# Performance work log

Measured on AMD Instinct MI355X. Metric: run time of the kernel, lower is better.

## Reference

```python
import jax, jax.numpy as jnp
import numpy as np

IMG = 64
NZ = 100
ENC_H = 800
DEC_H = 1600
IN_SZ = IMG * IMG  # 4096
D_ENC_IN = 2 * IN_SZ * 3 + DEC_H  # 26176


def setup_inputs() -> dict:
    key = jax.random.key(0)
    ks = jax.random.split(key, 12)
    B, T = 64, 10
    s = 0.02  # weight init scale to keep gates in sane range
    return {
        "x": jax.random.uniform(ks[0], (B, 3, IMG, IMG), jnp.float32),
        "noise": jax.random.normal(ks[1], (T, B, NZ), jnp.float32),
        "W_ih_mu": jax.random.normal(ks[2], (4 * ENC_H, D_ENC_IN), jnp.float32) * s,
        "W_hh_mu": jax.random.normal(ks[3], (4 * ENC_H, ENC_H), jnp.float32) * s,
        "b_mu": jnp.zeros((4 * ENC_H,), jnp.float32),
        "W_ih_lv": jax.random.normal(ks[4], (4 * ENC_H, D_ENC_IN), jnp.float32) * s,
        "W_hh_lv": jax.random.normal(ks[5], (4 * ENC_H, ENC_H), jnp.float32) * s,
        "b_lv": jnp.zeros((4 * ENC_H,), jnp.float32),
        "W_mu_fc": jax.random.normal(ks[6], (NZ, ENC_H), jnp.float32) * s,
        "b_mu_fc": jnp.zeros((NZ,), jnp.float32),
        "W_lv_fc": jax.random.normal(ks[7], (NZ, ENC_H), jnp.float32) * s,
        "b_lv_fc": jnp.zeros((NZ,), jnp.float32),
        "W_ih_dec": jax.random.normal(ks[8], (4 * DEC_H, NZ), jnp.float32) * s,
        "W_hh_dec": jax.random.normal(ks[9], (4 * DEC_H, DEC_H), jnp.float32) * s,
        "b_dec": jnp.zeros((4 * DEC_H,), jnp.float32),
        "W_write": jax.random.normal(ks[10], (3 * IN_SZ, DEC_H), jnp.float32) * s,
        "b_write": jnp.zeros((3 * IN_SZ,), jnp.float32),
        "T": T,
    }


def _lstm_cell(xin, h, c, W_ih, W_hh, b):
    # torch LSTMCell: gates ordered i, f, g, o
    g = xin @ W_ih.T + h @ W_hh.T + b
    i, f, gg, o = jnp.split(g, 4, axis=1)
    c_new = jax.nn.sigmoid(f) * c + jax.nn.sigmoid(i) * jnp.tanh(gg)
    h_new = jax.nn.sigmoid(o) * jnp.tanh(c_new)
    return h_new, c_new


def reference(x, noise, W_ih_mu, W_hh_mu, b_mu, W_ih_lv, W_hh_lv, b_lv,
              W_mu_fc, b_mu_fc, W_lv_fc, b_lv_fc,
              W_ih_dec, W_hh_dec, b_dec, W_write, b_write, T):
    B = x.shape[0]
    x_flat = x.reshape(B, -1)  # [B, 3*64*64]
    init = (
        jnp.zeros((B, 3, IMG, IMG), x.dtype),   # canvas c
        jnp.zeros((B, ENC_H), x.dtype), jnp.zeros((B, ENC_H), x.dtype),  # h_mu, c_mu
        jnp.zeros((B, ENC_H), x.dtype), jnp.zeros((B, ENC_H), x.dtype),  # h_lv, c_lv
        jnp.zeros((B, DEC_H), x.dtype), jnp.zeros((B, DEC_H), x.dtype),  # h_dec, c_dec
    )

    def step(carry, eps):
        c, h_mu, c_mu, h_lv, c_lv, h_dec, c_dec = carry
        sb = jax.nn.sigmoid(c)
        x_hat = (x - sb).reshape(B, -1)
        enc_in = jnp.concatenate([x_flat, x_hat, h_dec], axis=1)  # [B, 26176]
        h_mu, c_mu = _lstm_cell(enc_in, h_mu, c_mu, W_ih_mu, W_hh_mu, b_mu)
        mu = jax.nn.relu(h_mu @ W_mu_fc.T + b_mu_fc)
        h_lv, c_lv = _lstm_cell(enc_in, h_lv, c_lv, W_ih_lv, W_hh_lv, b_lv)
        logvar = jax.nn.relu(h_lv @ W_lv_fc.T + b_lv_fc)
        z = eps * jnp.exp(0.5 * logvar) + mu
        h_dec, c_dec = _lstm_cell(z, h_dec, c_dec, W_ih_dec, W_hh_dec, b_dec)
        wr = (h_dec @ W_write.T + b_write).reshape(B, 3, IMG, IMG)
        c = c + wr
        return (c, h_mu, c_mu, h_lv, c_lv, h_dec, c_dec), (mu, logvar)

    (c, *_), (mu_t, logvar_t) = jax.lax.scan(step, init, noise)
    return jax.nn.sigmoid(c), mu_t, logvar_t
```

## Files before the change

kernel.cpp:

```cpp
#include <hip/hip_runtime.h>

typedef __attribute__((ext_vector_type(8))) short bf16x8;
typedef __attribute__((ext_vector_type(4))) float f32x4;
typedef __attribute__((ext_vector_type(4))) int i32x4;
typedef unsigned int u32;

#define B_SZ   64
#define IMGSZ  12288
#define ENC_H  800
#define DEC_H  1600
#define NZ     100
#define NENC   6400
#define KHH    832
#define KDEC   1728
#define GSZ    (B_SZ*NENC)
#define SLICES 7
#define G0SL   8

#define WQMUL    1008.0f
#define SCALE_I8 (-1.0f/(254.0f*1008.0f))

__device__ __forceinline__ unsigned short f2bf(float f){
  unsigned u = __float_as_uint(f);
  u += 0x7fffu + ((u >> 16) & 1u);
  return (unsigned short)(u >> 16);
}
__device__ __forceinline__ float bf2f(unsigned short h){
  return __uint_as_float(((unsigned)h) << 16);
}
__device__ __forceinline__ float sigf(float x){ return 1.f/(1.f + __expf(-x)); }
__device__ __forceinline__ ushort4 cv4(float4 v){
  ushort4 o; o.x=f2bf(v.x); o.y=f2bf(v.y); o.z=f2bf(v.z); o.w=f2bf(v.w); return o;
}
__device__ __forceinline__ unsigned q4(float4 v){
  int a = __float2int_rn(fminf(fmaxf(v.x*WQMUL, -127.f), 127.f));
  int b = __float2int_rn(fminf(fmaxf(v.y*WQMUL, -127.f), 127.f));
  int c = __float2int_rn(fminf(fmaxf(v.z*WQMUL, -127.f), 127.f));
  int d = __float2int_rn(fminf(fmaxf(v.w*WQMUL, -127.f), 127.f));
  return (a&255) | ((b&255)<<8) | ((c&255)<<16) | ((d&255)<<24);
}

__device__ __forceinline__ void gllb(const void* g, void* l){
  __builtin_amdgcn_global_load_lds((const __attribute__((address_space(1))) u32*)g,
                                   (__attribute__((address_space(3))) u32*)l, 16, 0, 0);
}

__device__ __forceinline__ void gemm_lds3(const unsigned short* __restrict__ A, int lda, int k0,
                                          const unsigned short* __restrict__ Bpk, size_t bchunk0,
                                          int nchb, unsigned short (*sm)[4096], f32x4 acc[4])
{
  const int tid = threadIdx.x;
  const int lane = tid & 63, w = tid >> 6;
  const int l15 = lane & 15, lg = lane >> 4;
  const int l8 = lane >> 3, l7 = lane & 7;

  const unsigned short* gA0 = A + (size_t)(w*16 + l8)*lda + k0 + (l7 ^ l8)*8;
  const unsigned short* gA1 = gA0 + (size_t)8*lda;
  const unsigned short* gB0 = Bpk + bchunk0*4096 + w*1024 + lane*8;

#pragma unroll
  for (int m = 0; m < 4; ++m) acc[m] = (f32x4){0.f,0.f,0.f,0.f};

  gllb(gA0, &sm[0][(w*2+0)*512]);
  gllb(gA1, &sm[0][(w*2+1)*512]);
  gllb(gB0,       &sm[1][w*1024]);
  gllb(gB0 + 512, &sm[1][w*1024 + 512]);
  if (1 < nchb){
    gllb(gA0 + 64, &sm[2][(w*2+0)*512]);
    gllb(gA1 + 64, &sm[2][(w*2+1)*512]);
    gllb(gB0 + 4096,       &sm[3][w*1024]);
    gllb(gB0 + 4096 + 512, &sm[3][w*1024 + 512]);
  }

  int cur = 0, nxt = 2;
  for (int c = 0; c < nchb; ++c){
    if (c + 1 < nchb) { asm volatile("s_waitcnt vmcnt(4)" ::: "memory"); }
    else              { asm volatile("s_waitcnt vmcnt(0)" ::: "memory"); }
    asm volatile("s_barrier" ::: "memory");
    const unsigned short* sa = sm[cur*2];
    const unsigned short* sb = sm[cur*2 + 1];
#pragma unroll
    for (int h = 0; h < 2; ++h){
      const int su8 = ((h*4 + lg) ^ (l15 & 7)) * 8;
      bf16x8 bfr = *(const bf16x8*)&sb[(w*16 + l15)*64 + su8];
#pragma unroll
      for (int m = 0; m < 4; ++m){
        bf16x8 afr = *(const bf16x8*)&sa[(m*16 + l15)*64 + su8];
        acc[m] = __builtin_amdgcn_mfma_f32_16x16x32_bf16(afr, bfr, acc[m], 0,0,0);
      }
    }
    if (c + 2 < nchb){
      const size_t ao = (size_t)(c+2)*64, bo = (size_t)(c+2)*4096;
      gllb(gA0 + ao, &sm[nxt*2][(w*2+0)*512]);
      gllb(gA1 + ao, &sm[nxt*2][(w*2+1)*512]);
      gllb(gB0 + bo,       &sm[nxt*2+1][w*1024]);
      gllb(gB0 + bo + 512, &sm[nxt*2+1][w*1024 + 512]);
    }
    cur = (cur==2) ? 0 : cur+1;
    nxt = (nxt==2) ? 0 : nxt+1;
  }
}

__device__ __forceinline__ void gemm_i8(const signed char* __restrict__ A, int lda, int k0,
                                        const signed char* __restrict__ Bpk, size_t bch0,
                                        int nch, unsigned char* sm, i32x4 acc[4])
{
  const int tid = threadIdx.x;
  const int lane = tid & 63, w = tid >> 6;
  const int l15 = lane & 15, lg = lane >> 4;

  const int rp = lane >> 3, un = lane & 7;
  const int swz = un ^ (rp & 7);
  const int rloc = rp*2 + ((swz >> 2) & 1);
  const int uA = swz & 3;
  const signed char* gA = A + (size_t)(w*16 + rloc)*lda + k0 + uA*16;
  const signed char* gB = Bpk + bch0*4096 + w*1024 + lane*16;

#pragma unroll
  for (int m = 0; m < 4; ++m) acc[m] = (i32x4){0,0,0,0};

  {
    gllb(gA, sm + 0*8192 + w*1024 + lane*16);
    gllb(gB, sm + 0*8192 + 4096 + w*1024 + lane*16);
    if (1 < nch){
      gllb(gA + 64,   sm + 1*8192 + w*1024 + lane*16);
      gllb(gB + 4096, sm + 1*8192 + 4096 + w*1024 + lane*16);
    }
  }

  const int rB = w*16 + l15;
  const int offB = 4096 + (rB>>1)*128 + (((((rB&1)<<2) + lg) ^ ((rB>>1)&7))*16);

  int cur = 0, nxt = 2;
  for (int c = 0; c < nch; ++c){
    if (c + 1 < nch) { asm volatile("s_waitcnt vmcnt(2)" ::: "memory"); }
    else             { asm volatile("s_waitcnt vmcnt(0)" ::: "memory"); }
    asm volatile("s_barrier" ::: "memory");
    const unsigned char* s = sm + cur*8192;
    i32x4 bfr = *(const i32x4*)(s + offB);
#pragma unroll
    for (int m = 0; m < 4; ++m){
      int rA = m*16 + l15;
      i32x4 afr = *(const i32x4*)(s + (rA>>1)*128 + (((((rA&1)<<2) + lg) ^ ((rA>>1)&7))*16));
      acc[m] = __builtin_amdgcn_mfma_i32_16x16x64_i8(afr, bfr, acc[m], 0, 0, 0);
    }
    if (c + 2 < nch){
      gllb(gA + (size_t)(c+2)*64,   sm + nxt*8192 + w*1024 + lane*16);
      gllb(gB + (size_t)(c+2)*4096, sm + nxt*8192 + 4096 + w*1024 + lane*16);
    }
    cur = (cur==2) ? 0 : cur+1;
    nxt = (nxt==2) ? 0 : nxt+1;
  }
}

__device__ __forceinline__ void store_out1(f32x4 acc[4], float* __restrict__ Out,
                                           int ldo, int col0){
  const int lane = threadIdx.x & 63, w = threadIdx.x >> 6;
  const int l15 = lane & 15, lg = lane >> 4;
  int col = col0 + w*16 + l15;
#pragma unroll
  for (int m = 0; m < 4; ++m)
#pragma unroll
    for (int j = 0; j < 4; ++j)
      Out[(size_t)(m*16 + lg*4 + j)*ldo + col] = acc[m][j];
}

__device__ __forceinline__ void store_i8(i32x4 acc[4], float* __restrict__ Out,
                                         int ldo, int col0){
  const int lane = threadIdx.x & 63, w = threadIdx.x >> 6;
  const int l15 = lane & 15, lg = lane >> 4;
  int col = col0 + w*16 + l15;
#pragma unroll
  for (int m = 0; m < 4; ++m)
#pragma unroll
    for (int j = 0; j < 4; ++j)
      Out[(size_t)(m*16 + lg*4 + j)*ldo + col] = SCALE_I8 * (float)acc[m][j];
}


__global__ __launch_bounds__(256) void k_pack_encmain(const float* __restrict__ Wihmu,
                                                      const float* __restrict__ Wihlv,
                                                      unsigned short* __restrict__ wab,
                                                      unsigned char* __restrict__ wi8,
                                                      float* __restrict__ csPart){
  __shared__ float cs[256];
  int ch = blockIdx.x;
  int cb = blockIdx.y;
  int t = threadIdx.x;
  int r = t >> 2, seg = t & 3;
  int col = cb*64 + r;
  const float4* src = (col < 3200) ? ((const float4*)Wihmu + (size_t)col*6544)
                                   : ((const float4*)Wihlv + (size_t)(col-3200)*6544);
  int k4b = ch*16 + seg*4;
  float4 va[4], vb[4];
#pragma unroll
  for (int i = 0; i < 4; ++i){ va[i] = src[k4b+i]; vb[i] = src[3072 + k4b + i]; }

  ushort4* wabT = (ushort4*)wab + ((size_t)cb*192 + ch)*1024;
#pragma unroll
  for (int d = 0; d < 2; ++d){
    int u16 = seg*2 + d;
    int su = u16 ^ (r & 7);
    float4 s0, s1;
    s0.x=va[2*d].x+vb[2*d].x;   s0.y=va[2*d].y+vb[2*d].y;
    s0.z=va[2*d].z+vb[2*d].z;   s0.w=va[2*d].w+vb[2*d].w;
    s1.x=va[2*d+1].x+vb[2*d+1].x; s1.y=va[2*d+1].y+vb[2*d+1].y;
    s1.z=va[2*d+1].z+vb[2*d+1].z; s1.w=va[2*d+1].w+vb[2*d+1].w;
    wabT[r*16 + su*2 + 0] = cv4(s0);
    wabT[r*16 + su*2 + 1] = cv4(s1);
  }

  unsigned char* wi8T = wi8 + ((size_t)cb*192 + ch)*4096;
  int unit = (((r&1)<<2) + seg) ^ ((r>>1) & 7);
  uint4 pk;
  pk.x = q4(vb[0]); pk.y = q4(vb[1]); pk.z = q4(vb[2]); pk.w = q4(vb[3]);
  *(uint4*)(wi8T + (r>>1)*128 + unit*16) = pk;

  float s = 0.f;
#pragma unroll
  for (int i = 0; i < 4; ++i) s += vb[i].x + vb[i].y + vb[i].z + vb[i].w;
  cs[t] = s;
  __syncthreads();
  if (seg == 0)
    csPart[((size_t)col)*192 + ch] = cs[t] + cs[t+1] + cs[t+2] + cs[t+3];
}

__global__ __launch_bounds__(256) void k_csred(const float* __restrict__ csPart,
                                               float* __restrict__ colsum){
  unsigned col = blockIdx.x*blockDim.x + threadIdx.x;
  if (col >= NENC) return;
  const float* p = csPart + (size_t)col*192;
  float s = 0.f;
#pragma unroll 8
  for (int ch = 0; ch < 192; ++ch) s += p[ch];
  colsum[col] = s;
}

__global__ __launch_bounds__(256) void k_pack_whc(const float* __restrict__ Wihmu,
                                                  const float* __restrict__ Wihlv,
                                                  unsigned short* __restrict__ whc){
  int ch = blockIdx.x;
  int cb = blockIdx.y;
  ushort4* whcT = (ushort4*)whc + ((size_t)cb*25 + ch)*1024;
#pragma unroll
  for (int q = 0; q < 4; ++q){
    int ou = q*256 + threadIdx.x;
    int r = ou >> 4, qq = ou & 15;
    int su = qq >> 1, half = qq & 1;
    int uu = su ^ (r & 7);
    int k4 = ch*16 + uu*2 + half;
    int col = cb*64 + r;
    const float4* src = (col < 3200) ? ((const float4*)Wihmu + (size_t)col*6544)
                                     : ((const float4*)Wihlv + (size_t)(col-3200)*6544);
    whcT[ou] = cv4(src[6144 + k4]);
  }
}

__global__ __launch_bounds__(256) void k_pack_whh(const float* __restrict__ Whhmu,
                                                  const float* __restrict__ Whhlv,
                                                  unsigned short* __restrict__ whh){
  int ch = blockIdx.x;
  int cb = blockIdx.y;
  ushort4* whhT = (ushort4*)whh + ((size_t)cb*13 + ch)*1024;
#pragma unroll
  for (int q = 0; q < 4; ++q){
    int ou = q*256 + threadIdx.x;
    int r = ou >> 4, qq = ou & 15;
    int su = qq >> 1, half = qq & 1;
    int uu = su ^ (r & 7);
    int k4 = ch*16 + uu*2 + half;
    int col = cb*64 + r;
    float4 v = {0.f,0.f,0.f,0.f};
    if (k4 < 200)
      v = (col < 3200) ? ((const float4*)Whhmu)[(size_t)col*200 + k4]
                       : ((const float4*)Whhlv)[(size_t)(col-3200)*200 + k4];
    whhT[ou] = cv4(v);
  }
}

__global__ __launch_bounds__(256) void k_pack_wdec(const float* __restrict__ Whhdec,
                                                   const float* __restrict__ Wihdec,
                                                   unsigned short* __restrict__ wdec){
  int ch = blockIdx.x;
  int cb = blockIdx.y;
  ushort4* wdecT = (ushort4*)wdec + ((size_t)cb*27 + ch)*1024;
#pragma unroll
  for (int q = 0; q < 4; ++q){
    int ou = q*256 + threadIdx.x;
    int r = ou >> 4, qq = ou & 15;
    int su = qq >> 1, half = qq & 1;
    int uu = su ^ (r & 7);
    int k4 = ch*16 + uu*2 + half;
    int pr = cb*64 + r;
    unsigned j = pr >> 2, g = pr & 3, srow = g*1600u + j;
    float4 v = {0.f,0.f,0.f,0.f};
    if (k4 < 400)      v = ((const float4*)Whhdec)[(size_t)srow*400 + k4];
    else if (k4 < 425) v = ((const float4*)Wihdec)[(size_t)srow*25 + (k4-400)];
    wdecT[ou] = cv4(v);
  }
}

__global__ __launch_bounds__(256) void k_pack_wwr(const float* __restrict__ Wwrite,
                                                  unsigned short* __restrict__ wwr){
  int ch = blockIdx.x;
  int cb = blockIdx.y;
  ushort4* wwrT = (ushort4*)wwr + ((size_t)cb*25 + ch)*1024;
#pragma unroll
  for (int q = 0; q < 4; ++q){
    int ou = q*256 + threadIdx.x;
    int r = ou >> 4, qq = ou & 15;
    int su = qq >> 1, half = qq & 1;
    int uu = su ^ (r & 7);
    int k4 = ch*16 + uu*2 + half;
    int p = cb*64 + r;
    wwrT[ou] = cv4(((const float4*)Wwrite)[(size_t)p*400 + k4]);
  }
}

#define M_FC   40000u
#define M_XBF  236608u
__global__ __launch_bounds__(256) void k_su_misc(const float* __restrict__ Wmufc,
                                                 const float* __restrict__ Wlvfc,
                                                 const float* __restrict__ x,
                                                 unsigned short* __restrict__ wfcmu,
                                                 unsigned short* __restrict__ wfclv,
                                                 unsigned short* __restrict__ xbf){
  unsigned i = blockIdx.x*blockDim.x + threadIdx.x;
  if (i >= M_XBF) return;
  if (i < M_FC){
    if (i < 20000u) ((ushort4*)wfcmu)[i] = cv4(((const float4*)Wmufc)[i]);
    else            ((ushort4*)wfclv)[i-20000u] = cv4(((const float4*)Wlvfc)[i-20000u]);
  } else {
    unsigned j = i - M_FC;
    ((ushort4*)xbf)[j] = cv4(((const float4*)x)[j]);
  }
}


__global__ __launch_bounds__(256) void k_g0(const unsigned short* __restrict__ xbf,
                                            const unsigned short* __restrict__ wab,
                                            float* __restrict__ gpart){
  __shared__ __align__(16) unsigned short smem[6][4096];
  int bid = blockIdx.x;
  int s = bid/100, cb = bid - s*100;
  f32x4 acc[4];
  gemm_lds3(xbf, IMGSZ, s*1536, wab, (size_t)cb*192 + s*24, 24, smem, acc);
  store_out1(acc, gpart + (size_t)s*GSZ, NENC, cb*64);
}

__global__ __launch_bounds__(256) void k_g0red(const float* __restrict__ gpart,
                                               float* __restrict__ g0){
  unsigned i = blockIdx.x*blockDim.x + threadIdx.x;
  if (i >= GSZ) return;
  float s = 0.f;
#pragma unroll
  for (int p = 0; p < G0SL; ++p) s += gpart[(size_t)p*GSZ + i];
  g0[i] = s;
}

__global__ __launch_bounds__(256) void k_enc(const signed char* __restrict__ ui8,
                                             const signed char* __restrict__ wi8,
                                             const unsigned short* __restrict__ uhd,
                                             const unsigned short* __restrict__ whc,
                                             const unsigned short* __restrict__ hmup,
                                             const unsigned short* __restrict__ hlvp,
                                             const unsigned short* __restrict__ whh,
                                             float* __restrict__ gpart){
  __shared__ __align__(16) unsigned char smem[49152];
  int bid = blockIdx.x;
  if (bid < 500){
    int s = bid/100, cb = bid - s*100;
    int ch0 = s*38 + (s < 2 ? s : 2);
    int nch = 38 + (s < 2 ? 1 : 0);
    i32x4 acc[4];
    gemm_i8(ui8, IMGSZ, ch0*64, wi8, (size_t)cb*192 + ch0, nch, smem, acc);
    store_i8(acc, gpart + (size_t)s*GSZ, NENC, cb*64);
  } else if (bid < 600){
    int cb = bid - 500;
    f32x4 acc[4];
    gemm_lds3(uhd, DEC_H, 0, whc, (size_t)cb*25, 25,
              (unsigned short (*)[4096])smem, acc);
    store_out1(acc, gpart + (size_t)5*GSZ, NENC, cb*64);
  } else {
    int cb = bid - 600;
    const unsigned short* A = (cb < 50) ? hmup : hlvp;
    f32x4 acc[4];
    gemm_lds3(A, KHH, 0, whh, (size_t)cb*13, 13,
              (unsigned short (*)[4096])smem, acc);
    store_out1(acc, gpart + (size_t)6*GSZ, NENC, cb*64);
  }
}

__global__ __launch_bounds__(512) void k_cell(const float* __restrict__ g0,
                                              const float* __restrict__ gpart,
                                              const float* __restrict__ colsum,
                                              const float* __restrict__ bmu,
                                              const float* __restrict__ blv,
                                              float* __restrict__ cmu,
                                              float* __restrict__ clv,
                                              unsigned short* __restrict__ hmup,
                                              unsigned short* __restrict__ hlvp,
                                              const unsigned short* __restrict__ wfcmu,
                                              const unsigned short* __restrict__ wfclv,
                                              const float* __restrict__ bmufc,
                                              const float* __restrict__ blvfc,
                                              const float* __restrict__ noise_t,
                                              float* __restrict__ outMu,
                                              float* __restrict__ outLv,
                                              unsigned short* __restrict__ u2z){
  __shared__ float hsh[1600];
  __shared__ float red[512];
  int b = blockIdx.x, tid = threadIdx.x;

  for (int uidx = tid; uidx < 1600; uidx += 512){
    int which = uidx >= 800;
    int j = uidx - which*800;
    const float* bias = which ? blv : bmu;
    int cbase = which*3200 + j;
    size_t rowoff = (size_t)b*NENC + cbase;
    float a0 = bias[j]       - 0.5f*colsum[cbase];
    float a1 = bias[800+j]   - 0.5f*colsum[cbase+800];
    float a2 = bias[1600+j]  - 0.5f*colsum[cbase+1600];
    float a3 = bias[2400+j]  - 0.5f*colsum[cbase+2400];
    const float* q = g0 + rowoff;
    a0 += q[0]; a1 += q[800]; a2 += q[1600]; a3 += q[2400];
#pragma unroll
    for (int s = 0; s < SLICES; ++s){
      const float* p = gpart + (size_t)s*GSZ + rowoff;
      a0 += p[0]; a1 += p[800]; a2 += p[1600]; a3 += p[2400];
    }
    float* C = which ? clv : cmu;
    float cold = C[(size_t)b*ENC_H + j];
    float cn = sigf(a1)*cold + sigf(a0)*tanhf(a2);
    float h  = sigf(a3)*tanhf(cn);
    C[(size_t)b*ENC_H + j] = cn;
    (which ? hlvp : hmup)[(size_t)b*KHH + j] = f2bf(h);
    hsh[uidx] = h;
  }
  __syncthreads();

  if (tid < 400){
    int o = tid >> 1, half = tid & 1;
    int ismu = o < 100;
    int row = ismu ? o : o - 100;
    const unsigned short* wrow = (ismu ? wfcmu : wfclv) + (size_t)row*ENC_H + half*400;
    const float* hbase = hsh + (ismu ? 0 : 800) + half*400;
    float s = 0.f;
#pragma unroll 4
    for (int k = 0; k < 100; ++k){
      ushort4 wv = ((const ushort4*)wrow)[k];
      s += bf2f(wv.x)*hbase[k*4]   + bf2f(wv.y)*hbase[k*4+1]
         + bf2f(wv.z)*hbase[k*4+2] + bf2f(wv.w)*hbase[k*4+3];
    }
    red[tid] = s;
  }
  __syncthreads();
  if (tid < 200){
    int o = tid; int ismu = o < 100; int row = ismu ? o : o - 100;
    float s = red[2*o] + red[2*o+1] + (ismu ? bmufc[row] : blvfc[row]);
    s = fmaxf(s, 0.f);
    if (ismu) outMu[(size_t)b*NZ + row] = s;
    else      outLv[(size_t)b*NZ + row] = s;
    hsh[o] = s;
  }
  __syncthreads();
  if (tid < 100){
    float mu = hsh[tid], lv = hsh[100 + tid];
    float z = noise_t[(size_t)b*NZ + tid]*__expf(0.5f*lv) + mu;
    u2z[(size_t)b*KDEC + DEC_H + tid] = f2bf(z);
  }
}

__global__ __launch_bounds__(256) void k_dec(const unsigned short* __restrict__ u2r,
                                             const unsigned short* __restrict__ wdec,
                                             const float* __restrict__ bdec,
                                             float* __restrict__ cdec,
                                             unsigned short* __restrict__ uhd,
                                             unsigned short* __restrict__ u2w){
  __shared__ __align__(16) unsigned short smem[6][4096];
  int bid = blockIdx.x;
  f32x4 acc[4];
  gemm_lds3(u2r, KDEC, 0, wdec, (size_t)bid*27, 27, smem, acc);
  __syncthreads();
  float* lds = (float*)&smem[0][0];
  const int lane = threadIdx.x & 63;
  const int wave = threadIdx.x >> 6;
  const int l15 = lane & 15, lg = lane >> 4;
#pragma unroll
  for (int m = 0; m < 4; ++m)
#pragma unroll
    for (int j = 0; j < 4; ++j)
      lds[(m*16 + lg*4 + j)*65 + wave*16 + l15] = acc[m][j];
  __syncthreads();
#pragma unroll
  for (int p = 0; p < 4; ++p){
    int idx = threadIdx.x + p*256;
    int b = idx & 63, jj = idx >> 6;
    const float* g4 = &lds[b*65 + jj*4];
    int j = bid*16 + jj;
    float gi = g4[0] + bdec[j];
    float gf = g4[1] + bdec[DEC_H + j];
    float gg = g4[2] + bdec[2*DEC_H + j];
    float go = g4[3] + bdec[3*DEC_H + j];
    float cold = cdec[(size_t)b*DEC_H + j];
    float cn = sigf(gf)*cold + sigf(gi)*tanhf(gg);
    float h  = sigf(go)*tanhf(cn);
    cdec[(size_t)b*DEC_H + j] = cn;
    unsigned short hb = f2bf(h);
    u2w[(size_t)b*KDEC + j] = hb;
    uhd[(size_t)b*DEC_H + j] = hb;
  }
}

__global__ __launch_bounds__(256) void k_write(const unsigned short* __restrict__ u2,
                                               const unsigned short* __restrict__ wwr,
                                               const float* __restrict__ bwr,
                                               float* __restrict__ canvas,
                                               signed char* __restrict__ ui8){
  __shared__ __align__(16) unsigned short smem[6][4096];
  f32x4 acc[4];
  gemm_lds3(u2, KDEC, 0, wwr, (size_t)blockIdx.x*25, 25, smem, acc);
  const int lane = threadIdx.x & 63;
  const int wave = threadIdx.x >> 6;
  const int l15 = lane & 15, lg = lane >> 4;
  int col = blockIdx.x*64 + wave*16 + l15;
#pragma unroll
  for (int m = 0; m < 4; ++m){
#pragma unroll
    for (int j = 0; j < 4; ++j){
      int row = m*16 + lg*4 + j;
      float cv = canvas[(size_t)row*IMGSZ + col] + acc[m][j] + bwr[col];
      canvas[(size_t)row*IMGSZ + col] = cv;
      ui8[(size_t)row*IMGSZ + col] =
        (signed char)__float2int_rn((sigf(cv) - 0.5f)*254.f);
    }
  }
}

__global__ __launch_bounds__(256) void k_final(const float* __restrict__ canvas,
                                               float* __restrict__ out){
  unsigned i = blockIdx.x*blockDim.x + threadIdx.x;
  if (i < (unsigned)(B_SZ*IMGSZ)) out[i] = sigf(canvas[i]);
}

constexpr size_t SZ_WAB    = (size_t)NENC*IMGSZ*2;
constexpr size_t SZ_WI8    = (size_t)NENC*IMGSZ;
constexpr size_t SZ_WHC    = (size_t)NENC*DEC_H*2;
constexpr size_t SZ_WHH    = (size_t)NENC*KHH*2;
constexpr size_t SZ_WDEC   = (size_t)NENC*KDEC*2;
constexpr size_t SZ_WWR    = (size_t)IMGSZ*DEC_H*2;
constexpr size_t SZ_WFC    = (size_t)NZ*ENC_H*2;
constexpr size_t SZ_XBF    = (size_t)B_SZ*IMGSZ*2;
constexpr size_t SZ_CSPART = (size_t)NENC*192*4;
constexpr size_t SZ_CSUM   = (size_t)NENC*4;
constexpr size_t SZ_G0     = (size_t)GSZ*4;
constexpr size_t SZ_GPART  = (size_t)G0SL*GSZ*4;
constexpr size_t SZ_CANVAS = (size_t)B_SZ*IMGSZ*4;
constexpr size_t SZ_CMU    = (size_t)B_SZ*ENC_H*4;
constexpr size_t SZ_CDEC   = (size_t)B_SZ*DEC_H*4;
constexpr size_t SZ_HP     = (size_t)B_SZ*KHH*2;
constexpr size_t SZ_UHD    = (size_t)B_SZ*DEC_H*2;
constexpr size_t SZ_U2     = (size_t)B_SZ*KDEC*2;
constexpr size_t SZ_UI8    = (size_t)B_SZ*IMGSZ;

constexpr size_t OFF_WAB    = 0;
constexpr size_t OFF_WI8    = OFF_WAB    + SZ_WAB;
constexpr size_t OFF_WHC    = OFF_WI8    + SZ_WI8;
constexpr size_t OFF_WHH    = OFF_WHC    + SZ_WHC;
constexpr size_t OFF_WDEC   = OFF_WHH    + SZ_WHH;
constexpr size_t OFF_WWR    = OFF_WDEC   + SZ_WDEC;
constexpr size_t OFF_WFCMU  = OFF_WWR    + SZ_WWR;
constexpr size_t OFF_WFCLV  = OFF_WFCMU  + SZ_WFC;
constexpr size_t OFF_XBF    = OFF_WFCLV  + SZ_WFC;
constexpr size_t OFF_CSPART = OFF_XBF    + SZ_XBF;
constexpr size_t OFF_CSUM   = OFF_CSPART + SZ_CSPART;
constexpr size_t OFF_G0     = OFF_CSUM   + SZ_CSUM;
constexpr size_t OFF_GPART  = OFF_G0     + SZ_G0;
constexpr size_t OFF_CANVAS = OFF_GPART  + SZ_GPART;
constexpr size_t OFF_CMU    = OFF_CANVAS + SZ_CANVAS;
constexpr size_t OFF_CLV    = OFF_CMU    + SZ_CMU;
constexpr size_t OFF_CDEC   = OFF_CLV    + SZ_CMU;
constexpr size_t OFF_HMUP   = OFF_CDEC   + SZ_CDEC;
constexpr size_t OFF_HLVP   = OFF_HMUP   + SZ_HP;
constexpr size_t OFF_UHD    = OFF_HLVP   + SZ_HP;
constexpr size_t OFF_U2A    = OFF_UHD    + SZ_UHD;
constexpr size_t OFF_U2B    = OFF_U2A    + SZ_U2;
constexpr size_t OFF_UI8    = OFF_U2B    + SZ_U2;
constexpr size_t OFF_END    = OFF_UI8    + SZ_UI8;

extern "C" void kernel_launch(void* const* d_in, const int* in_sizes, int n_in,
                              void* d_out, int out_size, void* d_ws, size_t ws_size,
                              hipStream_t stream) {
  const float* x      = (const float*)d_in[0];
  const float* noise  = (const float*)d_in[1];
  const float* Wihmu  = (const float*)d_in[2];
  const float* Whhmu  = (const float*)d_in[3];
  const float* bmu    = (const float*)d_in[4];
  const float* Wihlv  = (const float*)d_in[5];
  const float* Whhlv  = (const float*)d_in[6];
  const float* blv    = (const float*)d_in[7];
  const float* Wmufc  = (const float*)d_in[8];
  const float* bmufc  = (const float*)d_in[9];
  const float* Wlvfc  = (const float*)d_in[10];
  const float* blvfc  = (const float*)d_in[11];
  const float* Wihdec = (const float*)d_in[12];
  const float* Whhdec = (const float*)d_in[13];
  const float* bdec   = (const float*)d_in[14];
  const float* Wwrite = (const float*)d_in[15];
  const float* bwrite = (const float*)d_in[16];
  int T = in_sizes[1] / (B_SZ*NZ);

  if (ws_size < OFF_END) return;

  char* ws = (char*)d_ws;
  unsigned short* wab   = (unsigned short*)(ws + OFF_WAB);
  unsigned char*  wi8   = (unsigned char*)(ws + OFF_WI8);
  unsigned short* whc   = (unsigned short*)(ws + OFF_WHC);
  unsigned short* whh   = (unsigned short*)(ws + OFF_WHH);
  unsigned short* wdec  = (unsigned short*)(ws + OFF_WDEC);
  unsigned short* wwr   = (unsigned short*)(ws + OFF_WWR);
  unsigned short* wfcmu = (unsigned short*)(ws + OFF_WFCMU);
  unsigned short* wfclv = (unsigned short*)(ws + OFF_WFCLV);
  unsigned short* xbf   = (unsigned short*)(ws + OFF_XBF);
  float* csPart = (float*)(ws + OFF_CSPART);
  float* colsum = (float*)(ws + OFF_CSUM);
  float* g0     = (float*)(ws + OFF_G0);
  float* gpart  = (float*)(ws + OFF_GPART);
  float* canvas = (float*)(ws + OFF_CANVAS);
  float* cmu    = (float*)(ws + OFF_CMU);
  float* clv    = (float*)(ws + OFF_CLV);
  float* cdec   = (float*)(ws + OFF_CDEC);
  unsigned short* hmup = (unsigned short*)(ws + OFF_HMUP);
  unsigned short* hlvp = (unsigned short*)(ws + OFF_HLVP);
  unsigned short* uhd  = (unsigned short*)(ws + OFF_UHD);
  unsigned short* u2[2] = { (unsigned short*)(ws + OFF_U2A),
                            (unsigned short*)(ws + OFF_U2B) };
  signed char* ui8 = (signed char*)(ws + OFF_UI8);

  float* out = (float*)d_out;
  float* outMu = out + (size_t)B_SZ*IMGSZ;
  float* outLv = outMu + (size_t)T*B_SZ*NZ;

  dim3 blk(256);

  k_pack_encmain<<<dim3(192, 100), blk, 0, stream>>>(Wihmu, Wihlv, wab, wi8, csPart);
  k_pack_whc<<<dim3(25, 100), blk, 0, stream>>>(Wihmu, Wihlv, whc);
  k_pack_whh<<<dim3(13, 100), blk, 0, stream>>>(Whhmu, Whhlv, whh);
  k_pack_wdec<<<dim3(27, 100), blk, 0, stream>>>(Whhdec, Wihdec, wdec);
  k_pack_wwr<<<dim3(25, 192), blk, 0, stream>>>(Wwrite, wwr);
  k_csred<<<(NENC + 255)/256, blk, 0, stream>>>(csPart, colsum);
  hipMemsetAsync(ws + OFF_CANVAS, 0, OFF_END - OFF_CANVAS, stream);
  k_su_misc<<<(M_XBF + 255)/256, blk, 0, stream>>>(Wmufc, Wlvfc, x, wfcmu, wfclv, xbf);

  k_g0<<<800, blk, 0, stream>>>(xbf, wab, gpart);
  k_g0red<<<GSZ/256, blk, 0, stream>>>(gpart, g0);

  for (int t = 0; t < T; ++t){
    unsigned short* u2r = u2[t & 1];
    unsigned short* u2w = u2[(t + 1) & 1];
    k_enc<<<700, blk, 0, stream>>>(ui8, (const signed char*)wi8, uhd, whc,
                                   hmup, hlvp, whh, gpart);
    k_cell<<<B_SZ, 512, 0, stream>>>(g0, gpart, colsum, bmu, blv, cmu, clv,
                                     hmup, hlvp, wfcmu, wfclv, bmufc, blvfc,
                                     noise + (size_t)t*B_SZ*NZ,
                                     outMu + (size_t)t*B_SZ*NZ,
                                     outLv + (size_t)t*B_SZ*NZ, u2r);
    k_dec<<<100, blk, 0, stream>>>(u2r, wdec, bdec, cdec, uhd, u2w);
    k_write<<<IMGSZ/64, blk, 0, stream>>>(u2w, wwr, bwrite, canvas, ui8);
  }

  k_final<<<(B_SZ*IMGSZ)/256, blk, 0, stream>>>(canvas, out);
}
```

Before: 946.2 us.

## Stage encoder and write-weight packing through LDS with pipelined global-to-LDS loads

Rewrites the encoder-input and write-weight packing kernels so each block handles several k-chunks. Loads go global→LDS through a triple-buffered pipeline paced by explicit vmcnt waits and barriers, and each lane reads coalesced along a weight row instead of strided float4 loads. The column-sum partials shrink from 192 to 24 per column, which cuts the reduction work. This adds inline-asm synchronisation complexity and LDS use that may lower occupancy.

```diff
diff --git a/kernel.cpp b/kernel.cpp
--- a/kernel.cpp
+++ b/kernel.cpp
@@ -178,61 +178,131 @@
 }
 
 
-__global__ __launch_bounds__(256) void k_pack_encmain(const float* __restrict__ Wihmu,
-                                                      const float* __restrict__ Wihlv,
-                                                      unsigned short* __restrict__ wab,
-                                                      unsigned char* __restrict__ wi8,
-                                                      float* __restrict__ csPart){
-  __shared__ float cs[256];
-  int ch = blockIdx.x;
-  int cb = blockIdx.y;
-  int t = threadIdx.x;
-  int r = t >> 2, seg = t & 3;
-  int col = cb*64 + r;
-  const float4* src = (col < 3200) ? ((const float4*)Wihmu + (size_t)col*6544)
-                                   : ((const float4*)Wihlv + (size_t)(col-3200)*6544);
-  int k4b = ch*16 + seg*4;
-  float4 va[4], vb[4];
-#pragma unroll
-  for (int i = 0; i < 4; ++i){ va[i] = src[k4b+i]; vb[i] = src[3072 + k4b + i]; }
-
-  ushort4* wabT = (ushort4*)wab + ((size_t)cb*192 + ch)*1024;
-#pragma unroll
-  for (int d = 0; d < 2; ++d){
-    int u16 = seg*2 + d;
-    int su = u16 ^ (r & 7);
+__global__ __launch_bounds__(256) void k_pack_enc2(const float* __restrict__ Wihmu,
+                                                   const float* __restrict__ Wihlv,
+                                                   unsigned short* __restrict__ wab,
+                                                   unsigned char* __restrict__ wi8,
+                                                   float* __restrict__ csPart){
+  __shared__ __align__(16) float lds[3][4096];
+  const int tid = threadIdx.x;
+  const int lane = tid & 63, w = tid >> 6;
+  const int cb = blockIdx.y, bx = blockIdx.x;
+  const int ch0 = bx*8;
+  const int gcol_l = cb*64 + lane;
+  const float* row_l = (gcol_l < 3200) ? Wihmu + (size_t)gcol_l*26176
+                                       : Wihlv + (size_t)(gcol_l-3200)*26176;
+  const int r = tid >> 2, q = tid & 3;
+  const int gcol_r = cb*64 + r;
+
+  const int nsub = 16;
+  float csacc = 0.f;
+
+#define ENC2_STAGE(S, B) {                                             \
+    int ch_ = ch0 + ((S)>>1), p_ = (S)&1;                              \
+    const float* bA = row_l + ch_*64 + p_*32;                          \
+    float* dA = &lds[B][0];                                            \
+    float* dB = &lds[B][2048];                                         \
+    gllb(bA + (0*4 + w)*4,         dA + (0*4 + w)*256);                \
+    gllb(bA + (1*4 + w)*4,         dA + (1*4 + w)*256);                \
+    gllb(bA + 12288 + (0*4 + w)*4, dB + (0*4 + w)*256);                \
+    gllb(bA + 12288 + (1*4 + w)*4, dB + (1*4 + w)*256);                \
+  }
+
+  ENC2_STAGE(0, 0);
+  ENC2_STAGE(1, 1);
+
+  for (int s = 0; s < nsub; ++s){
+    if (s == 0)            { asm volatile("s_waitcnt vmcnt(4)" ::: "memory"); }
+    else if (s + 1 < nsub) { asm volatile("s_waitcnt vmcnt(7)" ::: "memory"); }
+    else                   { asm volatile("s_waitcnt vmcnt(0)" ::: "memory"); }
+    asm volatile("s_barrier" ::: "memory");
+
+    const int b = s % 3;
+    const int ch = ch0 + (s>>1), p = s&1;
+    const float* sA = &lds[b][0];
+    const float* sB = &lds[b][2048];
+    float4 a0 = *(const float4*)&sA[(q*2+0)*256 + r*4];
+    float4 a1 = *(const float4*)&sA[(q*2+1)*256 + r*4];
+    float4 b0 = *(const float4*)&sB[(q*2+0)*256 + r*4];
+    float4 b1 = *(const float4*)&sB[(q*2+1)*256 + r*4];
+
+    ushort4* wabT = (ushort4*)wab + ((size_t)cb*192 + ch)*1024;
+    unsigned char* wi8T = wi8 + ((size_t)cb*192 + ch)*4096;
+    int u16g = p*4 + q;
+    int su = u16g ^ (r & 7);
     float4 s0, s1;
-    s0.x=va[2*d].x+vb[2*d].x;   s0.y=va[2*d].y+vb[2*d].y;
-    s0.z=va[2*d].z+vb[2*d].z;   s0.w=va[2*d].w+vb[2*d].w;
-    s1.x=va[2*d+1].x+vb[2*d+1].x; s1.y=va[2*d+1].y+vb[2*d+1].y;
-    s1.z=va[2*d+1].z+vb[2*d+1].z; s1.w=va[2*d+1].w+vb[2*d+1].w;
+    s0.x=a0.x+b0.x; s0.y=a0.y+b0.y; s0.z=a0.z+b0.z; s0.w=a0.w+b0.w;
+    s1.x=a1.x+b1.x; s1.y=a1.y+b1.y; s1.z=a1.z+b1.z; s1.w=a1.w+b1.w;
     wabT[r*16 + su*2 + 0] = cv4(s0);
     wabT[r*16 + su*2 + 1] = cv4(s1);
-  }
-
-  unsigned char* wi8T = wi8 + ((size_t)cb*192 + ch)*4096;
-  int unit = (((r&1)<<2) + seg) ^ ((r>>1) & 7);
-  uint4 pk;
-  pk.x = q4(vb[0]); pk.y = q4(vb[1]); pk.z = q4(vb[2]); pk.w = q4(vb[3]);
-  *(uint4*)(wi8T + (r>>1)*128 + unit*16) = pk;
-
-  float s = 0.f;
-#pragma unroll
-  for (int i = 0; i < 4; ++i) s += vb[i].x + vb[i].y + vb[i].z + vb[i].w;
-  cs[t] = s;
-  __syncthreads();
-  if (seg == 0)
-    csPart[((size_t)col)*192 + ch] = cs[t] + cs[t+1] + cs[t+2] + cs[t+3];
+    int u8 = p*2 + (q>>1);
+    int un = (((r&1)<<2) + u8) ^ ((r>>1) & 7);
+    uint2 pk; pk.x = q4(b0); pk.y = q4(b1);
+    *(uint2*)(wi8T + (r>>1)*128 + un*16 + (q&1)*8) = pk;
+
+    csacc += b0.x+b0.y+b0.z+b0.w + b1.x+b1.y+b1.z+b1.w;
+
+    if (s + 2 < nsub) ENC2_STAGE(s + 2, (s + 2) % 3);
+  }
+#undef ENC2_STAGE
+
+  csacc += __shfl_xor(csacc, 1);
+  csacc += __shfl_xor(csacc, 2);
+  if (q == 0) csPart[(size_t)gcol_r*24 + bx] = csacc;
+}
+
+__global__ __launch_bounds__(256) void k_pack_wwr2(const float* __restrict__ Wwrite,
+                                                   unsigned short* __restrict__ wwr){
+  __shared__ __align__(16) float lds[3][2048];
+  const int tid = threadIdx.x;
+  const int lane = tid & 63, w = tid >> 6;
+  const int cb = blockIdx.y, bx = blockIdx.x;
+  const int ch0 = bx*5;
+  const float* row_l = Wwrite + (size_t)(cb*64 + lane)*1600;
+  const int r = tid >> 2, q = tid & 3;
+  const int nsub = 10;
+
+#define WWR_STAGE(S, B) {                                              \
+    int ch_ = ch0 + ((S)>>1), p_ = (S)&1;                              \
+    const float* bA = row_l + ch_*64 + p_*32;                          \
+    float* dA = &lds[B][0];                                            \
+    gllb(bA + (0*4 + w)*4, dA + (0*4 + w)*256);                        \
+    gllb(bA + (1*4 + w)*4, dA + (1*4 + w)*256);                        \
+  }
+
+  WWR_STAGE(0, 0);
+  WWR_STAGE(1, 1);
+
+  for (int s = 0; s < nsub; ++s){
+    if (s == 0)            { asm volatile("s_waitcnt vmcnt(2)" ::: "memory"); }
+    else if (s + 1 < nsub) { asm volatile("s_waitcnt vmcnt(4)" ::: "memory"); }
+    else                   { asm volatile("s_waitcnt vmcnt(0)" ::: "memory"); }
+    asm volatile("s_barrier" ::: "memory");
+
+    const int b = s % 3;
+    const int ch = ch0 + (s>>1), p = s&1;
+    const float* sA = &lds[b][0];
+    float4 v0 = *(const float4*)&sA[(q*2+0)*256 + r*4];
+    float4 v1 = *(const float4*)&sA[(q*2+1)*256 + r*4];
+    ushort4* wwrT = (ushort4*)wwr + ((size_t)cb*25 + ch)*1024;
+    int u16g = p*4 + q;
+    int su = u16g ^ (r & 7);
+    wwrT[r*16 + su*2 + 0] = cv4(v0);
+    wwrT[r*16 + su*2 + 1] = cv4(v1);
+
+    if (s + 2 < nsub) WWR_STAGE(s + 2, (s + 2) % 3);
+  }
+#undef WWR_STAGE
 }
 
 __global__ __launch_bounds__(256) void k_csred(const float* __restrict__ csPart,
                                                float* __restrict__ colsum){
   unsigned col = blockIdx.x*blockDim.x + threadIdx.x;
   if (col >= NENC) return;
-  const float* p = csPart + (size_t)col*192;
+  const float* p = csPart + (size_t)col*24;
   float s = 0.f;
-#pragma unroll 8
-  for (int ch = 0; ch < 192; ++ch) s += p[ch];
+#pragma unroll
+  for (int ch = 0; ch < 24; ++ch) s += p[ch];
   colsum[col] = s;
 }
 
@@ -243,8 +313,8 @@
   int cb = blockIdx.y;
   ushort4* whcT = (ushort4*)whc + ((size_t)cb*25 + ch)*1024;
 #pragma unroll
-  for (int q = 0; q < 4; ++q){
-    int ou = q*256 + threadIdx.x;
+  for (int qq4 = 0; qq4 < 4; ++qq4){
+    int ou = qq4*256 + threadIdx.x;
     int r = ou >> 4, qq = ou & 15;
     int su = qq >> 1, half = qq & 1;
     int uu = su ^ (r & 7);
@@ -263,8 +333,8 @@
   int cb = blockIdx.y;
   ushort4* whhT = (ushort4*)whh + ((size_t)cb*13 + ch)*1024;
 #pragma unroll
-  for (int q = 0; q < 4; ++q){
-    int ou = q*256 + threadIdx.x;
+  for (int qq4 = 0; qq4 < 4; ++qq4){
+    int ou = qq4*256 + threadIdx.x;
     int r = ou >> 4, qq = ou & 15;
     int su = qq >> 1, half = qq & 1;
     int uu = su ^ (r & 7);
@@ -285,8 +355,8 @@
   int cb = blockIdx.y;
   ushort4* wdecT = (ushort4*)wdec + ((size_t)cb*27 + ch)*1024;
 #pragma unroll
-  for (int q = 0; q < 4; ++q){
-    int ou = q*256 + threadIdx.x;
+  for (int qq4 = 0; qq4 < 4; ++qq4){
+    int ou = qq4*256 + threadIdx.x;
     int r = ou >> 4, qq = ou & 15;
     int su = qq >> 1, half = qq & 1;
     int uu = su ^ (r & 7);
@@ -297,23 +367,6 @@
     if (k4 < 400)      v = ((const float4*)Whhdec)[(size_t)srow*400 + k4];
     else if (k4 < 425) v = ((const float4*)Wihdec)[(size_t)srow*25 + (k4-400)];
     wdecT[ou] = cv4(v);
-  }
-}
-
-__global__ __launch_bounds__(256) void k_pack_wwr(const float* __restrict__ Wwrite,
-                                                  unsigned short* __restrict__ wwr){
-  int ch = blockIdx.x;
-  int cb = blockIdx.y;
-  ushort4* wwrT = (ushort4*)wwr + ((size_t)cb*25 + ch)*1024;
-#pragma unroll
-  for (int q = 0; q < 4; ++q){
-    int ou = q*256 + threadIdx.x;
-    int r = ou >> 4, qq = ou & 15;
-    int su = qq >> 1, half = qq & 1;
-    int uu = su ^ (r & 7);
-    int k4 = ch*16 + uu*2 + half;
-    int p = cb*64 + r;
-    wwrT[ou] = cv4(((const float4*)Wwrite)[(size_t)p*400 + k4]);
   }
 }
 
@@ -551,7 +604,7 @@
 constexpr size_t SZ_WWR    = (size_t)IMGSZ*DEC_H*2;
 constexpr size_t SZ_WFC    = (size_t)NZ*ENC_H*2;
 constexpr size_t SZ_XBF    = (size_t)B_SZ*IMGSZ*2;
-constexpr size_t SZ_CSPART = (size_t)NENC*192*4;
+constexpr size_t SZ_CSPART = (size_t)NENC*24*4;
 constexpr size_t SZ_CSUM   = (size_t)NENC*4;
 constexpr size_t SZ_G0     = (size_t)GSZ*4;
 constexpr size_t SZ_GPART  = (size_t)G0SL*GSZ*4;
@@ -643,11 +696,11 @@
 
   dim3 blk(256);
 
-  k_pack_encmain<<<dim3(192, 100), blk, 0, stream>>>(Wihmu, Wihlv, wab, wi8, csPart);
+  k_pack_enc2<<<dim3(24, 100), blk, 0, stream>>>(Wihmu, Wihlv, wab, wi8, csPart);
   k_pack_whc<<<dim3(25, 100), blk, 0, stream>>>(Wihmu, Wihlv, whc);
   k_pack_whh<<<dim3(13, 100), blk, 0, stream>>>(Whhmu, Whhlv, whh);
   k_pack_wdec<<<dim3(27, 100), blk, 0, stream>>>(Whhdec, Wihdec, wdec);
-  k_pack_wwr<<<dim3(25, 192), blk, 0, stream>>>(Wwrite, wwr);
+  k_pack_wwr2<<<dim3(5, 192), blk, 0, stream>>>(Wwrite, wwr);
   k_csred<<<(NENC + 255)/256, blk, 0, stream>>>(csPart, colsum);
   hipMemsetAsync(ws + OFF_CANVAS, 0, OFF_END - OFF_CANVAS, stream);
   k_su_misc<<<(M_XBF + 255)/256, blk, 0, stream>>>(Wmufc, Wlvfc, x, wfcmu, wfclv, xbf);
```

Measured after the change: 1.013 ms. 7.0% more time.
